# Kernel optimization log

Measured on AMD Instinct MI355X. Metric: run time of the kernel, lower is better.

The kernel has to match this reference:

```python
import jax, jax.numpy as jnp
import numpy as np

WS = 16      # window_size
HEADS = 8    # num_heads
EPS = 1e-5   # LayerNorm eps (torch default)


def setup_inputs() -> dict:
    key = jax.random.key(0)
    ks = jax.random.split(key, 7)
    C = 256
    x = jax.random.normal(ks[0], (8, C, 128, 128), dtype=jnp.float32)
    # LayerNorm params (torch init: weight=1, bias=0)
    ln_w = jnp.ones((C,), jnp.float32)
    ln_b = jnp.zeros((C,), jnp.float32)
    # MultiheadAttention in_proj (3C x C) and out_proj (C x C), xavier-ish scale
    s = 1.0 / np.sqrt(C)
    w_qkv = jax.random.uniform(ks[1], (3 * C, C), jnp.float32, -s, s)
    b_qkv = jnp.zeros((3 * C,), jnp.float32)
    w_out = jax.random.uniform(ks[2], (C, C), jnp.float32, -s, s)
    b_out = jnp.zeros((C,), jnp.float32)
    return {"x": x, "ln_w": ln_w, "ln_b": ln_b, "w_qkv": w_qkv,
            "b_qkv": b_qkv, "w_out": w_out, "b_out": b_out}


def _layernorm(x, w, b):
    mu = jnp.mean(x, axis=-1, keepdims=True)
    var = jnp.mean(jnp.square(x - mu), axis=-1, keepdims=True)
    return (x - mu) * jax.lax.rsqrt(var + EPS) * w + b


def reference(x, ln_w, ln_b, w_qkv, b_qkv, w_out, b_out):
    B, C, H, W = x.shape
    pad_h = (WS - H % WS) % WS
    pad_w = (WS - W % WS) % WS
    if pad_h or pad_w:
        x_p = jnp.pad(x, ((0, 0), (0, 0), (0, pad_h), (0, pad_w)))
    else:
        x_p = x
    nH, nW = x_p.shape[2] // WS, x_p.shape[3] // WS
    T = WS * WS
    # window partition: [B,C,H,W] -> [B*nH*nW, T, C]
    win = x_p.reshape(B, C, nH, WS, nW, WS)
    win = win.transpose(0, 2, 4, 3, 5, 1).reshape(B * nH * nW, T, C)

    xn = _layernorm(win, ln_w, ln_b)
    # QKV projection: [N,T,3C]
    qkv = jnp.einsum('ntc,dc->ntd', xn, w_qkv) + b_qkv
    q, k, v = jnp.split(qkv, 3, axis=-1)
    hd = C // HEADS
    N = win.shape[0]
    q = q.reshape(N, T, HEADS, hd).transpose(0, 2, 1, 3)  # [N,h,T,hd]
    k = k.reshape(N, T, HEADS, hd).transpose(0, 2, 1, 3)
    v = v.reshape(N, T, HEADS, hd).transpose(0, 2, 1, 3)
    scores = jnp.einsum('nhqd,nhkd->nhqk', q, k) / jnp.sqrt(jnp.asarray(hd, q.dtype))
    attn = jax.nn.softmax(scores, axis=-1)
    ctx = jnp.einsum('nhqk,nhkd->nhqd', attn, v)
    ctx = ctx.transpose(0, 2, 1, 3).reshape(N, T, C)
    attn_out = jnp.einsum('ntc,dc->ntd', ctx, w_out) + b_out

    win = win + attn_out
    # window reverse: [N,T,C] -> [B,C,H,W]
    out = win.reshape(B, nH, nW, WS, WS, C)
    out = out.transpose(0, 5, 1, 3, 2, 4).reshape(B, C, nH * WS, nW * WS)
    return out[:, :, :H, :W]
```

## Files before the change

### kernel.cpp

```cpp
#include <hip/hip_runtime.h>
#include <hip/hip_bf16.h>

#define CD    256
#define HW_   16384
#define WSZ   16
#define TT    256
#define NWIN  512
#define NHEADS 8
#define HDIM  32

typedef __hip_bfloat16 bf16;
typedef unsigned short ushort_t;
typedef __attribute__((ext_vector_type(8))) short bf16x8;
typedef __attribute__((ext_vector_type(4))) float f32x4;

__device__ __forceinline__ ushort_t f2bu(float v) {
    union { bf16 b; ushort_t u; } cv; cv.b = __float2bfloat16(v); return cv.u;
}

__device__ __forceinline__ float fexp2(float x) {
#if __has_builtin(__builtin_amdgcn_exp2f)
    return __builtin_amdgcn_exp2f(x);
#else
    return exp2f(x);
#endif
}

__global__ __launch_bounds__(256)
void convw_kernel(const float* __restrict__ wq, const float* __restrict__ wo,
                  bf16* __restrict__ wqb, bf16* __restrict__ wob)
{
    int i = blockIdx.x * 256 + threadIdx.x;
    if (i < 3 * CD * CD) wqb[i] = __float2bfloat16(wq[i]);
    int j = i - 3 * CD * CD;
    if (j >= 0 && j < CD * CD) wob[j] = __float2bfloat16(wo[j]);
}

__global__ __launch_bounds__(64)
void ln_kernel(const float* __restrict__ x, const float* __restrict__ lnw,
               const float* __restrict__ lnb, bf16* __restrict__ xn)
{
    __shared__ bf16 buf[64][72];

    const int blk = blockIdx.x;
    const int n = blk >> 2, q4 = blk & 3;
    const int t = q4 * 64 + threadIdx.x;
    const int b = n >> 6, r = n & 63;
    const int h0 = (r >> 3) * WSZ, w0 = (r & 7) * WSZ;
    const int ty = t >> 4, tx = t & 15;
    const float* px = x + (size_t)b * CD * HW_ + (size_t)(h0 + ty) * 128 + (w0 + tx);

    float s = 0.f, ss = 0.f;
    for (int c = 0; c < CD; ++c) { float v = px[(size_t)c * HW_]; s += v; ss += v * v; }
    const float mean = s * (1.f / CD);
    const float var  = ss * (1.f / CD) - mean * mean;
    const float rstd = rsqrtf(fmaxf(var, 0.f) + 1e-5f);

    const size_t gbase = ((size_t)n * TT + (size_t)q4 * 64) * CD;
    for (int cb = 0; cb < 4; ++cb) {
        __syncthreads();
        #pragma unroll
        for (int c8 = 0; c8 < 8; ++c8) {
            union { int4 q; ushort_t u[8]; } pk;
            #pragma unroll
            for (int j = 0; j < 8; ++j) {
                int c = cb * 64 + c8 * 8 + j;
                float v = px[(size_t)c * HW_];
                pk.u[j] = f2bu((v - mean) * rstd * lnw[c] + lnb[c]);
            }
            *(int4*)&buf[threadIdx.x][c8 * 8] = pk.q;
        }
        __syncthreads();
        for (int sl = threadIdx.x; sl < 512; sl += 64) {
            int row = sl >> 3, ch = sl & 7;
            *(int4*)&xn[gbase + (size_t)row * CD + cb * 64 + ch * 8] =
                *(const int4*)&buf[row][ch * 8];
        }
    }
}

__global__ __launch_bounds__(256, 3)
void attn_kernel(const bf16* __restrict__ xn, const bf16* __restrict__ wqb,
                 const float* __restrict__ bqkv, bf16* __restrict__ ctx)
{
    const int n = blockIdx.x, h = blockIdx.y;
    const int tid = threadIdx.x;
    const int wave = tid >> 6, lane = tid & 63;
    const int l16 = lane & 15, q16 = lane >> 4;

    __shared__ bf16 qp[256][36];
    __shared__ bf16 ks[256][36];
    __shared__ bf16 vst[32][260];

    f32x4 acc[4][6];
    const f32x4 zero = {0.f, 0.f, 0.f, 0.f};
    #pragma unroll
    for (int mt = 0; mt < 4; ++mt)
        #pragma unroll
        for (int nt = 0; nt < 6; ++nt) acc[mt][nt] = zero;

    const bf16* arow[4];
    #pragma unroll
    for (int mt = 0; mt < 4; ++mt)
        arow[mt] = xn + ((size_t)n * TT + wave * 64 + mt * 16 + l16) * CD + q16 * 8;
    const bf16* brow[6];
    #pragma unroll
    for (int nt = 0; nt < 6; ++nt) {
        const int mat = nt >> 1;
        const int j = ((nt & 1) << 4) | l16;
        brow[nt] = wqb + ((size_t)(mat * CD + h * HDIM + j)) * CD + q16 * 8;
    }

    for (int kc = 0; kc < 8; ++kc) {
        bf16x8 af[4], bg[6];
        #pragma unroll
        for (int mt = 0; mt < 4; ++mt)
            af[mt] = *(const bf16x8*)(arow[mt] + kc * 32);
        #pragma unroll
        for (int nt = 0; nt < 6; ++nt)
            bg[nt] = *(const bf16x8*)(brow[nt] + kc * 32);
        #pragma unroll
        for (int mt = 0; mt < 4; ++mt)
            #pragma unroll
            for (int nt = 0; nt < 6; ++nt)
                acc[mt][nt] = __builtin_amdgcn_mfma_f32_16x16x32_bf16(
                                  af[mt], bg[nt], acc[mt][nt], 0, 0, 0);
    }

    const float qscale2 = 0.2550348683f;
    #pragma unroll
    for (int nt = 0; nt < 6; ++nt) {
        const int mat = nt >> 1;
        const int j = ((nt & 1) << 4) | l16;
        const float bias = bqkv[mat * CD + h * HDIM + j];
        #pragma unroll
        for (int mt = 0; mt < 4; ++mt)
            #pragma unroll
            for (int rr = 0; rr < 4; ++rr) {
                int tok = wave * 64 + mt * 16 + q16 * 4 + rr;
                float v = acc[mt][nt][rr] + bias;
                if (mat == 0)      qp[tok][j]  = __float2bfloat16(v * qscale2);
                else if (mat == 1) ks[tok][j]  = __float2bfloat16(v);
                else               vst[j][tok] = __float2bfloat16(v);
            }
    }
    __syncthreads();

    bf16x8 aq[4];
    #pragma unroll
    for (int mt = 0; mt < 4; ++mt)
        aq[mt] = *(const bf16x8*)&qp[wave * 64 + mt * 16 + l16][q16 * 8];

    bf16x8 onesf;
    #pragma unroll
    for (int j = 0; j < 8; ++j) onesf[j] = (short)0x3F80;

    f32x4 acc_o[4][2];
    f32x4 acc_l[4];
    #pragma unroll
    for (int mt = 0; mt < 4; ++mt) {
        acc_o[mt][0] = zero; acc_o[mt][1] = zero; acc_l[mt] = zero;
    }

    for (int kc = 0; kc < 8; ++kc) {
        bf16x8 kb0 = *(const bf16x8*)&ks[kc * 32 + l16][q16 * 8];
        bf16x8 kb1 = *(const bf16x8*)&ks[kc * 32 + 16 + l16][q16 * 8];
        #pragma unroll
        for (int mt = 0; mt < 4; ++mt) {
            f32x4 sc0 = __builtin_amdgcn_mfma_f32_16x16x32_bf16(aq[mt], kb0, zero, 0, 0, 0);
            f32x4 sc1 = __builtin_amdgcn_mfma_f32_16x16x32_bf16(aq[mt], kb1, zero, 0, 0, 0);
            #pragma unroll
            for (int rr = 0; rr < 4; ++rr) {
                float p0 = fexp2(sc0[rr]);
                float p1 = fexp2(sc1[rr]);
                int row = wave * 64 + mt * 16 + q16 * 4 + rr;
                qp[row][l16]      = __float2bfloat16(p0);
                qp[row][16 + l16] = __float2bfloat16(p1);
            }
        }
        bf16x8 vb0 = *(const bf16x8*)&vst[l16][kc * 32 + q16 * 8];
        bf16x8 vb1 = *(const bf16x8*)&vst[16 + l16][kc * 32 + q16 * 8];
        #pragma unroll
        for (int mt = 0; mt < 4; ++mt) {
            bf16x8 ap = *(const bf16x8*)&qp[wave * 64 + mt * 16 + l16][q16 * 8];
            acc_o[mt][0] = __builtin_amdgcn_mfma_f32_16x16x32_bf16(ap, vb0, acc_o[mt][0], 0, 0, 0);
            acc_o[mt][1] = __builtin_amdgcn_mfma_f32_16x16x32_bf16(ap, vb1, acc_o[mt][1], 0, 0, 0);
            acc_l[mt]    = __builtin_amdgcn_mfma_f32_16x16x32_bf16(ap, onesf, acc_l[mt], 0, 0, 0);
        }
    }

    #pragma unroll
    for (int mt = 0; mt < 4; ++mt)
        #pragma unroll
        for (int rr = 0; rr < 4; ++rr) {
            const float inv_l = 1.f / acc_l[mt][rr];
            int tok = wave * 64 + mt * 16 + q16 * 4 + rr;
            size_t base = ((size_t)n * TT + tok) * CD + h * HDIM;
            ctx[base + l16]      = __float2bfloat16(acc_o[mt][0][rr] * inv_l);
            ctx[base + 16 + l16] = __float2bfloat16(acc_o[mt][1][rr] * inv_l);
        }
}

__global__ __launch_bounds__(256, 2)
void proj_kernel(const bf16* __restrict__ ctx, const bf16* __restrict__ wob,
                 const float* __restrict__ bout, const float* __restrict__ x,
                 float* __restrict__ out)
{
    const int mb = blockIdx.x, nb = blockIdx.y;
    const int tid = threadIdx.x;
    const int wave = tid >> 6, lane = tid & 63;
    const int l16 = lane & 15, q16 = lane >> 4;
    const int rowbase = (wave >> 1) * 64, colbase = (wave & 1) * 64;

    __shared__ union {
        struct { bf16 a[128][64]; bf16 b[128][64]; } st;
        bf16 c[128][129];
    } u;

    f32x4 acc[4][4];
    const f32x4 zero = {0.f, 0.f, 0.f, 0.f};
    #pragma unroll
    for (int mt = 0; mt < 4; ++mt)
        #pragma unroll
        for (int nt = 0; nt < 4; ++nt) acc[mt][nt] = zero;

    const size_t m0 = (size_t)mb * 128;
    for (int kc = 0; kc < 4; ++kc) {
        __syncthreads();
        #pragma unroll
        for (int p = 0; p < 4; ++p) {
            int sl = p * 256 + tid;
            int row = sl >> 3, ch = sl & 7;
            *(int4*)&u.st.a[row][ch * 8] =
                *(const int4*)(ctx + (m0 + row) * CD + kc * 64 + ch * 8);
            *(int4*)&u.st.b[row][ch * 8] =
                *(const int4*)(wob + ((size_t)(nb * 128 + row)) * CD + kc * 64 + ch * 8);
        }
        __syncthreads();
        #pragma unroll
        for (int kt = 0; kt < 2; ++kt) {
            bf16x8 af[4], bg[4];
            #pragma unroll
            for (int mt = 0; mt < 4; ++mt)
                af[mt] = *(const bf16x8*)&u.st.a[rowbase + mt * 16 + l16][kt * 32 + q16 * 8];
            #pragma unroll
            for (int nt = 0; nt < 4; ++nt)
                bg[nt] = *(const bf16x8*)&u.st.b[colbase + nt * 16 + l16][kt * 32 + q16 * 8];
            #pragma unroll
            for (int mt = 0; mt < 4; ++mt)
                #pragma unroll
                for (int nt = 0; nt < 4; ++nt)
                    acc[mt][nt] = __builtin_amdgcn_mfma_f32_16x16x32_bf16(
                                      af[mt], bg[nt], acc[mt][nt], 0, 0, 0);
        }
    }
    __syncthreads();

    #pragma unroll
    for (int mt = 0; mt < 4; ++mt)
        #pragma unroll
        for (int nt = 0; nt < 4; ++nt)
            #pragma unroll
            for (int rr = 0; rr < 4; ++rr)
                u.c[rowbase + mt * 16 + q16 * 4 + rr][colbase + nt * 16 + l16] =
                    __float2bfloat16(acc[mt][nt][rr]);
    __syncthreads();

    const int dg = tid >> 5;
    const int t0 = (tid & 31) * 4;
    for (int p = 0; p < 16; ++p) {
        int d = p * 8 + dg;
        int c = nb * 128 + d;
        size_t g = m0 + t0;
        int n = (int)(g >> 8), wt = (int)(g & 255);
        int b = n >> 6, r = n & 63;
        int h0 = (r >> 3) * WSZ, w0 = (r & 7) * WSZ;
        int ty = wt >> 4, tx = wt & 15;
        size_t addr = (size_t)b * CD * HW_ + (size_t)c * HW_
                    + (size_t)(h0 + ty) * 128 + w0 + tx;
        float bias = bout[c];
        float4 xr = *(const float4*)(x + addr);
        float4 ov;
        ov.x = __bfloat162float(u.c[t0 + 0][d]) + bias + xr.x;
        ov.y = __bfloat162float(u.c[t0 + 1][d]) + bias + xr.y;
        ov.z = __bfloat162float(u.c[t0 + 2][d]) + bias + xr.z;
        ov.w = __bfloat162float(u.c[t0 + 3][d]) + bias + xr.w;
        *(float4*)(out + addr) = ov;
    }
}

extern "C" void kernel_launch(void* const* d_in, const int* in_sizes, int n_in,
                              void* d_out, int out_size, void* d_ws, size_t ws_size,
                              hipStream_t stream)
{
    const float* x   = (const float*)d_in[0];
    const float* lnw = (const float*)d_in[1];
    const float* lnb = (const float*)d_in[2];
    const float* wq  = (const float*)d_in[3];
    const float* bq  = (const float*)d_in[4];
    const float* wo  = (const float*)d_in[5];
    const float* bo  = (const float*)d_in[6];
    float* out = (float*)d_out;

    bf16* ctx = (bf16*)d_ws;
    bf16* wqb = ctx + (size_t)NWIN * TT * CD;
    bf16* wob = wqb + (size_t)3 * CD * CD;
    bf16* xn  = (bf16*)d_out;

    hipLaunchKernelGGL(convw_kernel, dim3(1024),         dim3(256), 0, stream, wq, wo, wqb, wob);
    hipLaunchKernelGGL(ln_kernel,    dim3(2048),         dim3(64),  0, stream, x, lnw, lnb, xn);
    hipLaunchKernelGGL(attn_kernel,  dim3(NWIN, NHEADS), dim3(256), 0, stream, xn, wqb, bq, ctx);
    hipLaunchKernelGGL(proj_kernel,  dim3(1024, 2),      dim3(256), 0, stream, ctx, wob, bo, x, out);
}
```

Baseline: 568.2 us.

## Rewrite LayerNorm kernel to load x once with float4 and split channels across waves

The LayerNorm kernel goes from 64 to 256 threads per block. Each thread now loads 16 channels times 4 pixels as float4 and keeps them in registers, so x is read once instead of twice (once for the statistics, once to normalize). Partial sums and sums of squares are reduced through shared memory, then the normalized bf16 values are staged in shared memory for coalesced writes. This aims to halve global reads and widen loads, at the cost of more registers per thread and extra block syncs.

```diff
diff --git a/kernel.cpp b/kernel.cpp
--- a/kernel.cpp
+++ b/kernel.cpp
@@ -36,46 +36,88 @@
     if (j >= 0 && j < CD * CD) wob[j] = __float2bfloat16(wo[j]);
 }
 
-__global__ __launch_bounds__(64)
+__global__ __launch_bounds__(256)
 void ln_kernel(const float* __restrict__ x, const float* __restrict__ lnw,
                const float* __restrict__ lnb, bf16* __restrict__ xn)
 {
-    __shared__ bf16 buf[64][72];
+    __shared__ union {
+        float2 part[16][66];
+        bf16 obuf[4][64][72];
+    } u;
+    __shared__ float2 stats[64];
 
     const int blk = blockIdx.x;
-    const int n = blk >> 2, q4 = blk & 3;
-    const int t = q4 * 64 + threadIdx.x;
+    const int n  = blk >> 2, q4 = blk & 3;
+    const int tid = threadIdx.x;
+    const int w  = tid >> 6, l = tid & 63;
+    const int cg = l >> 4, g = l & 15;
+
     const int b = n >> 6, r = n & 63;
     const int h0 = (r >> 3) * WSZ, w0 = (r & 7) * WSZ;
-    const int ty = t >> 4, tx = t & 15;
-    const float* px = x + (size_t)b * CD * HW_ + (size_t)(h0 + ty) * 128 + (w0 + tx);
-
-    float s = 0.f, ss = 0.f;
-    for (int c = 0; c < CD; ++c) { float v = px[(size_t)c * HW_]; s += v; ss += v * v; }
-    const float mean = s * (1.f / CD);
-    const float var  = ss * (1.f / CD) - mean * mean;
-    const float rstd = rsqrtf(fmaxf(var, 0.f) + 1e-5f);
-
-    const size_t gbase = ((size_t)n * TT + (size_t)q4 * 64) * CD;
-    for (int cb = 0; cb < 4; ++cb) {
-        __syncthreads();
-        #pragma unroll
-        for (int c8 = 0; c8 < 8; ++c8) {
-            union { int4 q; ushort_t u[8]; } pk;
-            #pragma unroll
-            for (int j = 0; j < 8; ++j) {
-                int c = cb * 64 + c8 * 8 + j;
-                float v = px[(size_t)c * HW_];
-                pk.u[j] = f2bu((v - mean) * rstd * lnw[c] + lnb[c]);
-            }
-            *(int4*)&buf[threadIdx.x][c8 * 8] = pk.q;
-        }
-        __syncthreads();
-        for (int sl = threadIdx.x; sl < 512; sl += 64) {
-            int row = sl >> 3, ch = sl & 7;
-            *(int4*)&xn[gbase + (size_t)row * CD + cb * 64 + ch * 8] =
-                *(const int4*)&buf[row][ch * 8];
-        }
+    const float* px = x + (size_t)b * CD * HW_
+                    + (size_t)(h0 + q4 * 4 + (g >> 2)) * 128 + (w0 + (g & 3) * 4);
+    const int c0 = w * 64 + cg * 16;
+
+    float4 xv[16];
+    float s[4] = {0.f, 0.f, 0.f, 0.f}, ss[4] = {0.f, 0.f, 0.f, 0.f};
+    #pragma unroll
+    for (int it = 0; it < 16; ++it) {
+        xv[it] = *(const float4*)(px + (size_t)(c0 + it) * HW_);
+        s[0] += xv[it].x; ss[0] += xv[it].x * xv[it].x;
+        s[1] += xv[it].y; ss[1] += xv[it].y * xv[it].y;
+        s[2] += xv[it].z; ss[2] += xv[it].z * xv[it].z;
+        s[3] += xv[it].w; ss[3] += xv[it].w * xv[it].w;
+    }
+    const int pc = w * 4 + cg;
+    #pragma unroll
+    for (int j = 0; j < 4; ++j)
+        u.part[pc][g * 4 + j] = make_float2(s[j], ss[j]);
+    __syncthreads();
+
+    if (tid < 64) {
+        float S = 0.f, SS = 0.f;
+        #pragma unroll
+        for (int p = 0; p < 16; ++p) {
+            float2 t = u.part[p][tid];
+            S += t.x; SS += t.y;
+        }
+        float mean = S * (1.f / CD);
+        float var  = SS * (1.f / CD) - mean * mean;
+        stats[tid] = make_float2(mean, rsqrtf(fmaxf(var, 0.f) + 1e-5f));
+    }
+    __syncthreads();
+
+    float2 st[4];
+    #pragma unroll
+    for (int j = 0; j < 4; ++j) st[j] = stats[g * 4 + j];
+
+    #pragma unroll
+    for (int it4 = 0; it4 < 4; ++it4) {
+        short4 pk[4];
+        #pragma unroll
+        for (int k = 0; k < 4; ++k) {
+            int c = c0 + it4 * 4 + k;
+            float wgt = lnw[c], bia = lnb[c];
+            float4 v = xv[it4 * 4 + k];
+            ushort_t u0 = f2bu((v.x - st[0].x) * st[0].y * wgt + bia);
+            ushort_t u1 = f2bu((v.y - st[1].x) * st[1].y * wgt + bia);
+            ushort_t u2 = f2bu((v.z - st[2].x) * st[2].y * wgt + bia);
+            ushort_t u3 = f2bu((v.w - st[3].x) * st[3].y * wgt + bia);
+            pk[0][k] = (short)u0; pk[1][k] = (short)u1;
+            pk[2][k] = (short)u2; pk[3][k] = (short)u3;
+        }
+        #pragma unroll
+        for (int j = 0; j < 4; ++j)
+            *(short4*)&u.obuf[w][4 * g + j][cg * 16 + it4 * 4] = pk[j];
+    }
+
+    const size_t gbase = ((size_t)n * TT + (size_t)q4 * 64) * CD + w * 64;
+    #pragma unroll
+    for (int it2 = 0; it2 < 8; ++it2) {
+        int tok = it2 * 8 + (l >> 3);
+        int k = l & 7;
+        *(int4*)(xn + gbase + (size_t)tok * CD + k * 8) =
+            *(const int4*)&u.obuf[w][tok][k * 8];
     }
 }
 
@@ -308,7 +350,7 @@
     bf16* xn  = (bf16*)d_out;
 
     hipLaunchKernelGGL(convw_kernel, dim3(1024),         dim3(256), 0, stream, wq, wo, wqb, wob);
-    hipLaunchKernelGGL(ln_kernel,    dim3(2048),         dim3(64),  0, stream, x, lnw, lnb, xn);
+    hipLaunchKernelGGL(ln_kernel,    dim3(2048),         dim3(256), 0, stream, x, lnw, lnb, xn);
     hipLaunchKernelGGL(attn_kernel,  dim3(NWIN, NHEADS), dim3(256), 0, stream, xn, wqb, bq, ctx);
     hipLaunchKernelGGL(proj_kernel,  dim3(1024, 2),      dim3(256), 0, stream, ctx, wob, bo, x, out);
 }
```

New measurement: 527.0 us. 1.08x faster.
